# Optimization experiments

Measured on AMD Instinct MI355X. Metric: run time of the kernel, lower is better.

Reference implementation:

```python
import jax, jax.numpy as jnp
import numpy as np
from jax.scipy.special import logsumexp

IN_FEATURES = 1024
N_CLASSES = 50257
CUTOFFS = [4000, 20000, N_CLASSES]  # includes final n_classes, as in the module
SHORTLIST = CUTOFFS[0]
N_CLUSTERS = len(CUTOFFS)
N = 8192


def setup_inputs() -> dict:
    key = jax.random.key(0)
    k1, k2, k3, k4, k5, k6 = jax.random.split(key, 6)
    inp = {
        "input": jax.random.normal(k1, (N, IN_FEATURES), dtype=jnp.float32),
        "target": jax.random.randint(k2, (N,), 0, N_CLASSES, dtype=jnp.int64)
        if jax.config.jax_enable_x64 else jax.random.randint(k2, (N,), 0, N_CLASSES, dtype=jnp.int32),
        # learned parameters
        "weight": jax.random.normal(k3, (N_CLASSES, IN_FEATURES), dtype=jnp.float32) * 0.02,
        "bias": jnp.zeros((N_CLASSES,), dtype=jnp.float32),
        "tail_vectors": jax.random.normal(k4, (N_CLUSTERS - 1, IN_FEATURES), dtype=jnp.float32) * 0.02,
        "tail_bias": jnp.zeros((N_CLUSTERS - 1,), dtype=jnp.float32),
    }
    return inp


def reference(input, target, weight, bias, tail_vectors, tail_bias):
    cutoff_values = [0] + CUTOFFS  # [0, 4000, 20000, 50257]

    # head = shortlist classes + one logit per tail cluster
    head_weight = jnp.concatenate([weight[:SHORTLIST], tail_vectors], axis=0)
    head_bias = jnp.concatenate([bias[:SHORTLIST], tail_bias], axis=0)
    head_logits = input @ head_weight.T + head_bias              # [N, shortlist + n_clusters-1]
    head_logprob = jax.nn.log_softmax(head_logits, axis=1)

    # which cluster each target falls in: 0 = shortlist, 1.. = tails
    boundaries = jnp.asarray(CUTOFFS[:-1])                        # [4000, 20000]
    cluster_id = jnp.searchsorted(boundaries, target, side="right")  # [N]

    # index into head distribution: target itself for shortlist, else cluster logit slot
    gather_inds = jnp.where(cluster_id == 0, target, SHORTLIST + cluster_id - 1)
    head_term = jnp.take_along_axis(head_logprob, gather_inds[:, None], axis=1)[:, 0]

    # per-row target logit against the full table (only used for tail rows)
    target_logit = jnp.sum(input * weight[target], axis=-1) + bias[target]  # [N]

    # tail clusters: within-cluster log-prob of the target = logit - logsumexp(cluster logits)
    tail_term = jnp.zeros_like(head_term)
    for i in range(1, N_CLUSTERS):
        lo, hi = cutoff_values[i], cutoff_values[i + 1]
        cluster_logits = input @ weight[lo:hi].T + bias[lo:hi]    # [N, hi-lo]
        lse = logsumexp(cluster_logits, axis=1)                   # [N]
        tail_term = jnp.where(cluster_id == i, target_logit - lse, tail_term)

    output = head_term + tail_term                                # [N] log-probs of targets
    loss = jnp.mean(-output)
    return output, loss
```

## Files before the change

### kernel.cpp

```cpp
#include <hip/hip_runtime.h>
#include <stddef.h>
#include <stdint.h>

#define IN_F      1024
#define SHORTLIST 4000
#define C1_LO     4000
#define C1_HI     20000
#define C2_HI     50257
#define NROWS     8192

#define WS_CNT1   0
#define WS_CNT2   1
#define WS_LOSS   2
#define WS_RL1    4
#define WS_RL2    (4 + 8192)
#define WS_SEH    (4 + 2*8192)
#define WS_SET    (WS_SEH + 8192)
#define WS_CAP    (WS_SET + 8192)
#define WS_WORDS  (WS_CAP + 8192)

#define WBF_OFF   (262144)
#define XBF_OFF   (WBF_OFF + 103219200)
#define XBF_BYTES ((size_t)NROWS * IN_F * 2)
#define WS_NEEDED (XBF_OFF + XBF_BYTES)

#define GRID_HEAD 512
#define GRID_T1   2048
#define GRID_T2   3840
#define GRID_ALL  (GRID_HEAD + GRID_T1 + GRID_T2)

typedef float          f32x4  __attribute__((ext_vector_type(4)));
typedef __bf16         bf16x8 __attribute__((ext_vector_type(8)));
typedef unsigned short us8    __attribute__((ext_vector_type(8)));
typedef unsigned short ushort_t;

__device__ __forceinline__ unsigned short f2bf(float f) {
    unsigned int u = __float_as_uint(f);
    u += 0x7fffu + ((u >> 16) & 1u);
    return (unsigned short)(u >> 16);
}

__device__ __forceinline__ void gl_lds16(const void* g, void* l) {
    __builtin_amdgcn_global_load_lds(
        (const __attribute__((address_space(1))) void*)g,
        (__attribute__((address_space(3))) void*)l, 16, 0, 0);
}

__global__ void init_ws_k(int* __restrict__ ws) {
    int i = blockIdx.x * 256 + threadIdx.x;
    if (i < WS_WORDS) {
        int v = (i >= WS_RL1 && i < WS_RL1 + 2*8192) ? -1 : 0;
        ws[i] = v;
    }
}

__global__ void compact_rows_k(const int* __restrict__ target, int* __restrict__ ws) {
    int row = blockIdx.x * 256 + threadIdx.x;
    if (row >= NROWS) return;
    int tg = target[row];
    if (tg >= C1_LO) {
        if (tg < C1_HI) {
            int p = atomicAdd(&ws[WS_CNT1], 1);
            ws[WS_RL1 + p] = row;
        } else {
            int p = atomicAdd(&ws[WS_CNT2], 1);
            ws[WS_RL2 + p] = row;
        }
    }
}

#define WCHUNKS ((C2_HI * IN_F) / 8)
#define XCHUNKS ((NROWS * IN_F) / 8)
__global__ void convert_bf16_k(const float* __restrict__ w_src,
                               ushort_t* __restrict__ w_dst,
                               const float* __restrict__ x_src,
                               ushort_t* __restrict__ x_dst) {
    int i = blockIdx.x * 256 + threadIdx.x;
    const float* p;
    ushort_t* d;
    if (i < WCHUNKS) { p = w_src + (size_t)i * 8; d = w_dst + (size_t)i * 8; }
    else {
        int j = i - WCHUNKS;
        if (j >= XCHUNKS) return;
        p = x_src + (size_t)j * 8; d = x_dst + (size_t)j * 8;
    }
    f32x4 x0 = *(const f32x4*)p;
    f32x4 x1 = *(const f32x4*)(p + 4);
    us8 o;
    o[0] = f2bf(x0[0]); o[1] = f2bf(x0[1]); o[2] = f2bf(x0[2]); o[3] = f2bf(x0[3]);
    o[4] = f2bf(x1[0]); o[5] = f2bf(x1[1]); o[6] = f2bf(x1[2]); o[7] = f2bf(x1[3]);
    *(us8*)d = o;
}

__launch_bounds__(256, 3)
__global__ void gemm_lse_fused_k(const ushort_t* __restrict__ Xbf,
                                 const ushort_t* __restrict__ Wbf,
                                 const float* __restrict__ bias,
                                 const int*   __restrict__ target,
                                 int*   __restrict__ wsI,
                                 float* __restrict__ wsF)
{
    const int bid = blockIdx.x;
    int rs, cg, cbase, C, cnt;
    const int* rowlist;
    float* sumexp;
    if (bid < GRID_HEAD) {
        rs = bid & 63; cg = bid >> 6;
        cbase = 0; C = SHORTLIST; rowlist = nullptr; cnt = NROWS;
        sumexp = wsF + WS_SEH;
    } else if (bid < GRID_HEAD + GRID_T1) {
        int b = bid - GRID_HEAD;
        rs = b & 63; cg = b >> 6;
        cbase = C1_LO; C = C1_HI - C1_LO; rowlist = wsI + WS_RL1; cnt = wsI[WS_CNT1];
        sumexp = wsF + WS_SET;
    } else {
        int b = bid - (GRID_HEAD + GRID_T1);
        rs = b & 63; cg = b >> 6;
        cbase = C1_HI; C = C2_HI - C1_HI; rowlist = wsI + WS_RL2; cnt = wsI[WS_CNT2];
        sumexp = wsF + WS_SET;
    }
    const int r0 = rs * 128;
    if (r0 >= cnt) return;
    float* capture = wsF + WS_CAP;

    __shared__ ushort_t As[128 * 64];
    __shared__ ushort_t Bs[128 * 64];
    __shared__ int   orig_s[128];
    __shared__ int   tgt_s[128];
    __shared__ float part[256];

    const int tid = threadIdx.x;
    part[tid] = 0.f;
    if (tid < 128) {
        int idx  = r0 + tid;
        int orig = (idx < cnt) ? (rowlist ? rowlist[idx] : idx) : -1;
        orig_s[tid] = orig;
        tgt_s[tid]  = (orig >= 0) ? target[orig] : -1;
    }
    __syncthreads();

    const int lane = tid & 63;
    const int wave = tid >> 6;
    const int wm = wave >> 1, wn = wave & 1;
    const int q = lane >> 4, s = lane & 15;

    const int lrow  = lane >> 3;
    const int chunk = (lane & 7) ^ lrow;
    const ushort_t* aptr[4];
    ushort_t* alds[4];
    ushort_t* blds[4];
    int brow[4];
#pragma unroll
    for (int i = 0; i < 4; ++i) {
        int t  = wave * 4 + i;
        int rt = t * 8 + lrow;
        int orig = orig_s[rt]; if (orig < 0) orig = 0;
        aptr[i] = Xbf + (size_t)orig * IN_F + chunk * 8;
        alds[i] = &As[t * 512];
        blds[i] = &Bs[t * 512];
        brow[i] = rt;
    }

    int aoff[4], boff[4];
#pragma unroll
    for (int i = 0; i < 4; ++i) {
        aoff[i] = (wm * 64 + i * 16 + s) * 64;
        boff[i] = (wn * 64 + i * 16 + s) * 64;
    }
    const int slot0 = (q ^ (s & 7)) * 8;
    const int slot1 = slot0 ^ (4 * 8);

    for (int ct = 0; ct < 4; ++ct) {
        const int c0 = (cg * 4 + ct) * 128;
        if (c0 >= C) break;

        const ushort_t* bptr[4];
#pragma unroll
        for (int i = 0; i < 4; ++i) {
            int c = c0 + brow[i]; if (c >= C) c = C - 1;
            bptr[i] = Wbf + (size_t)(cbase + c) * IN_F + chunk * 8;
        }

        f32x4 acc[4][4];
#pragma unroll
        for (int mi = 0; mi < 4; ++mi)
#pragma unroll
            for (int ni = 0; ni < 4; ++ni) acc[mi][ni] = (f32x4)0.f;

        for (int k0 = 0; k0 < IN_F; k0 += 64) {
            __syncthreads();
#pragma unroll
            for (int i = 0; i < 4; ++i) {
                gl_lds16(aptr[i] + k0, alds[i]);
                gl_lds16(bptr[i] + k0, blds[i]);
            }
            __syncthreads();

#pragma unroll
            for (int ks = 0; ks < 2; ++ks) {
                const int sl = ks ? slot1 : slot0;
                bf16x8 av[4], bv[4];
#pragma unroll
                for (int i = 0; i < 4; ++i) {
                    av[i] = *(const bf16x8*)&As[aoff[i] + sl];
                    bv[i] = *(const bf16x8*)&Bs[boff[i] + sl];
                }
#pragma unroll
                for (int mi = 0; mi < 4; ++mi)
#pragma unroll
                    for (int ni = 0; ni < 4; ++ni)
                        acc[mi][ni] = __builtin_amdgcn_mfma_f32_16x16x32_bf16(
                            av[mi], bv[ni], acc[mi][ni], 0, 0, 0);
            }
        }

        float bias_v[4];
#pragma unroll
        for (int ni = 0; ni < 4; ++ni) {
            int cgl = c0 + wn * 64 + ni * 16 + s;
            bias_v[ni] = (cgl < C) ? bias[cbase + cgl] : 0.f;
        }
#pragma unroll
        for (int mi = 0; mi < 4; ++mi) {
#pragma unroll
            for (int r = 0; r < 4; ++r) {
                int rl   = wm * 64 + mi * 16 + q * 4 + r;
                int orig = orig_s[rl];
                int tg   = tgt_s[rl];
                float sum = 0.f;
#pragma unroll
                for (int ni = 0; ni < 4; ++ni) {
                    int cgl = c0 + wn * 64 + ni * 16 + s;
                    float logit = acc[mi][ni][r] + bias_v[ni];
                    bool valid = (cgl < C) && (orig >= 0);
                    float e = valid ? __expf(logit) : 0.f;
                    sum += e;
                    if (valid && (cbase + cgl == tg)) capture[orig] = logit;
                }
                sum += __shfl_xor(sum, 1, 64);
                sum += __shfl_xor(sum, 2, 64);
                sum += __shfl_xor(sum, 4, 64);
                sum += __shfl_xor(sum, 8, 64);
                if (s == 0 && orig >= 0) part[wn * 128 + rl] += sum;
            }
        }
    }

    __syncthreads();
    if (tid < 128) {
        int orig = orig_s[tid];
        if (orig >= 0) {
            float tot = part[tid] + part[128 + tid];
            atomicAdd(&sumexp[orig], tot);
        }
    }
}

__launch_bounds__(256)
__global__ void gemm_lse_k(const float* __restrict__ input,
                           const float* __restrict__ weight,
                           const float* __restrict__ bias,
                           const int*   __restrict__ target,
                           const int*   __restrict__ rowlist,
                           const int*   __restrict__ cnt_ptr,
                           int fixed_cnt,
                           int class_base, int C,
                           float* __restrict__ sumexp,
                           float* __restrict__ capture)
{
    const int cnt = cnt_ptr ? *cnt_ptr : fixed_cnt;
    const int r0  = blockIdx.x * 128;
    if (r0 >= cnt) return;
    const int c0  = blockIdx.y * 128;

    __shared__ unsigned short As[128 * 40];
    __shared__ unsigned short Bs[128 * 40];
    __shared__ int   orig_s[128];
    __shared__ int   tgt_s[128];
    __shared__ float bias_s[128];

    const int tid = threadIdx.x;
    if (tid < 128) {
        int idx  = r0 + tid;
        int orig = -1;
        if (idx < cnt) orig = rowlist ? rowlist[idx] : idx;
        orig_s[tid] = orig;
        tgt_s[tid]  = (orig >= 0) ? target[orig] : -1;
        int c = c0 + tid;
        bias_s[tid] = (c < C) ? bias[class_base + c] : 0.f;
    }

    const int lane = tid & 63;
    const int wave = tid >> 6;
    const int wm = wave >> 1, wn = wave & 1;
    const int q = lane >> 4, s = lane & 15;

    int aoff[4], boff[4];
#pragma unroll
    for (int i = 0; i < 4; ++i) {
        aoff[i] = (wm * 64 + i * 16 + s) * 40 + q * 8;
        boff[i] = (wn * 64 + i * 16 + s) * 40 + q * 8;
    }

    f32x4 acc[4][4];
#pragma unroll
    for (int mi = 0; mi < 4; ++mi)
#pragma unroll
        for (int ni = 0; ni < 4; ++ni) acc[mi][ni] = (f32x4)0.f;

    for (int k0 = 0; k0 < IN_F; k0 += 32) {
        __syncthreads();
#pragma unroll
        for (int i = 0; i < 2; ++i) {
            int sg  = tid + i * 256;
            int row = sg >> 2;
            int sk  = (sg & 3) << 3;
            {
                int orig = orig_s[row];
                float v[8];
                if (orig >= 0) {
                    const float* p = input + (size_t)orig * IN_F + k0 + sk;
                    f32x4 x0 = *(const f32x4*)p;
                    f32x4 x1 = *(const f32x4*)(p + 4);
                    v[0]=x0[0]; v[1]=x0[1]; v[2]=x0[2]; v[3]=x0[3];
                    v[4]=x1[0]; v[5]=x1[1]; v[6]=x1[2]; v[7]=x1[3];
                } else {
#pragma unroll
                    for (int j = 0; j < 8; ++j) v[j] = 0.f;
                }
                us8 o;
#pragma unroll
                for (int j = 0; j < 8; ++j) o[j] = f2bf(v[j]);
                *(us8*)&As[row * 40 + sk] = o;
            }
            {
                int c = c0 + row;
                float v[8];
                if (c < C) {
                    const float* p = weight + (size_t)(class_base + c) * IN_F + k0 + sk;
                    f32x4 x0 = *(const f32x4*)p;
                    f32x4 x1 = *(const f32x4*)(p + 4);
                    v[0]=x0[0]; v[1]=x0[1]; v[2]=x0[2]; v[3]=x0[3];
                    v[4]=x1[0]; v[5]=x1[1]; v[6]=x1[2]; v[7]=x1[3];
                } else {
#pragma unroll
                    for (int j = 0; j < 8; ++j) v[j] = 0.f;
                }
                us8 o;
#pragma unroll
                for (int j = 0; j < 8; ++j) o[j] = f2bf(v[j]);
                *(us8*)&Bs[row * 40 + sk] = o;
            }
        }
        __syncthreads();

        bf16x8 av[4], bv[4];
#pragma unroll
        for (int i = 0; i < 4; ++i) {
            av[i] = *(const bf16x8*)&As[aoff[i]];
            bv[i] = *(const bf16x8*)&Bs[boff[i]];
        }
#pragma unroll
        for (int mi = 0; mi < 4; ++mi)
#pragma unroll
            for (int ni = 0; ni < 4; ++ni)
                acc[mi][ni] = __builtin_amdgcn_mfma_f32_16x16x32_bf16(
                    av[mi], bv[ni], acc[mi][ni], 0, 0, 0);
    }

#pragma unroll
    for (int mi = 0; mi < 4; ++mi) {
#pragma unroll
        for (int r = 0; r < 4; ++r) {
            int rl   = wm * 64 + mi * 16 + q * 4 + r;
            int orig = orig_s[rl];
            int tg   = tgt_s[rl];
            float sum = 0.f;
#pragma unroll
            for (int ni = 0; ni < 4; ++ni) {
                int cl = wn * 64 + ni * 16 + s;
                int cg = c0 + cl;
                float logit = acc[mi][ni][r] + bias_s[cl];
                bool valid = (cg < C) && (orig >= 0);
                float e = valid ? __expf(logit) : 0.f;
                sum += e;
                if (valid && (class_base + cg == tg)) capture[orig] = logit;
            }
            sum += __shfl_xor(sum, 1, 64);
            sum += __shfl_xor(sum, 2, 64);
            sum += __shfl_xor(sum, 4, 64);
            sum += __shfl_xor(sum, 8, 64);
            if (s == 0 && orig >= 0) atomicAdd(&sumexp[orig], sum);
        }
    }
}

__global__ void combine_k(const float* __restrict__ input,
                          const int*   __restrict__ target,
                          const float* __restrict__ tv,
                          const float* __restrict__ tb,
                          const float* __restrict__ sumexp_head,
                          const float* __restrict__ sumexp_tail,
                          const float* __restrict__ capture,
                          float* __restrict__ out,
                          float* __restrict__ loss_accum)
{
    const int wave = threadIdx.x >> 6, lane = threadIdx.x & 63;
    const int row = blockIdx.x * 4 + wave;
    if (row >= NROWS) return;

    const float* x  = input + (size_t)row * IN_F + lane * 16;
    const float* p0 = tv + lane * 16;
    const float* p1 = tv + IN_F + lane * 16;
    float d0 = 0.f, d1 = 0.f;
#pragma unroll
    for (int i = 0; i < 16; i += 4) {
        f32x4 xv = *(const f32x4*)(x  + i);
        f32x4 a  = *(const f32x4*)(p0 + i);
        f32x4 b  = *(const f32x4*)(p1 + i);
        d0 += xv[0]*a[0] + xv[1]*a[1] + xv[2]*a[2] + xv[3]*a[3];
        d1 += xv[0]*b[0] + xv[1]*b[1] + xv[2]*b[2] + xv[3]*b[3];
    }
#pragma unroll
    for (int m = 32; m; m >>= 1) {
        d0 += __shfl_xor(d0, m, 64);
        d1 += __shfl_xor(d1, m, 64);
    }
    if (lane == 0) {
        float t0 = d0 + tb[0];
        float t1 = d1 + tb[1];
        int tg  = target[row];
        int cid = (tg < C1_LO) ? 0 : ((tg < C1_HI) ? 1 : 2);
        float se_head  = sumexp_head[row] + __expf(t0) + __expf(t1);
        float lse_head = __logf(se_head);
        float head_num = (cid == 0) ? capture[row] : ((cid == 1) ? t0 : t1);
        float o = head_num - lse_head;
        if (cid != 0) o += capture[row] - __logf(sumexp_tail[row]);
        out[row] = o;
        atomicAdd(loss_accum, o);
    }
}

__global__ void finalize_k(const float* __restrict__ loss_accum, float* __restrict__ out) {
    out[NROWS] = -loss_accum[0] * (1.0f / NROWS);
}

extern "C" void kernel_launch(void* const* d_in, const int* in_sizes, int n_in,
                              void* d_out, int out_size, void* d_ws, size_t ws_size,
                              hipStream_t stream) {
    const float* input  = (const float*)d_in[0];
    const int*   target = (const int*)  d_in[1];
    const float* weight = (const float*)d_in[2];
    const float* bias   = (const float*)d_in[3];
    const float* tv     = (const float*)d_in[4];
    const float* tb     = (const float*)d_in[5];
    float* out = (float*)d_out;
    int*   wsI = (int*)d_ws;
    float* wsF = (float*)d_ws;

    init_ws_k<<<dim3((WS_WORDS + 255) / 256), 256, 0, stream>>>(wsI);
    compact_rows_k<<<dim3(NROWS / 256), 256, 0, stream>>>(target, wsI);

    const bool fast = ws_size >= (size_t)WS_NEEDED;

    if (fast) {
        ushort_t* Wbf = (ushort_t*)((char*)d_ws + WBF_OFF);
        ushort_t* Xbf = (ushort_t*)((char*)d_ws + XBF_OFF);

        convert_bf16_k<<<dim3((WCHUNKS + XCHUNKS + 255) / 256), 256, 0, stream>>>(
            weight, Wbf, input, Xbf);

        gemm_lse_fused_k<<<dim3(GRID_ALL), 256, 0, stream>>>(
            Xbf, Wbf, bias, target, wsI, wsF);
    } else {
        gemm_lse_k<<<dim3(NROWS / 128, (SHORTLIST + 127) / 128), 256, 0, stream>>>(
            input, weight, bias, target,
            nullptr, nullptr, NROWS,
            0, SHORTLIST,
            wsF + WS_SEH, wsF + WS_CAP);
        gemm_lse_k<<<dim3(NROWS / 128, (C1_HI - C1_LO + 127) / 128), 256, 0, stream>>>(
            input, weight, bias, target,
            wsI + WS_RL1, wsI + WS_CNT1, 0,
            C1_LO, C1_HI - C1_LO,
            wsF + WS_SET, wsF + WS_CAP);
        gemm_lse_k<<<dim3(NROWS / 128, (C2_HI - C1_HI + 127) / 128), 256, 0, stream>>>(
            input, weight, bias, target,
            wsI + WS_RL2, wsI + WS_CNT2, 0,
            C1_HI, C2_HI - C1_HI,
            wsF + WS_SET, wsF + WS_CAP);
    }

    combine_k<<<dim3(NROWS / 4), 256, 0, stream>>>(
        input, target, tv, tb,
        wsF + WS_SEH, wsF + WS_SET, wsF + WS_CAP,
        out, wsF + WS_LOSS);

    finalize_k<<<1, 1, 0, stream>>>(wsF + WS_LOSS, out);
}
```

Before: 1.189 ms.

## Double-buffer LDS tiles with vmcnt-gated prefetch in the fused GEMM-LSE kernel

Replaces the single 64-wide K tile, which needed two syncthreads per step, with two 32-wide LDS buffers pairs. The next K slice is loaded asynchronously via global_load_lds while MFMAs consume the current one, using s_waitcnt vmcnt(4) and raw barriers instead of full drains. The LDS swizzle and the thread-to-row mapping are reworked for the 32-element row stride. The aim is to hide global-load latency behind matrix math, at the cost of more barriers per unit of K and a hand-tuned wait count that must match the number of loads issued.

```diff
diff --git a/kernel.cpp b/kernel.cpp
--- a/kernel.cpp
+++ b/kernel.cpp
@@ -45,6 +45,10 @@
         (const __attribute__((address_space(1))) void*)g,
         (__attribute__((address_space(3))) void*)l, 16, 0, 0);
 }
+
+#define VMCNT4() asm volatile("s_waitcnt vmcnt(4)" ::: "memory")
+#define VMCNT0() asm volatile("s_waitcnt vmcnt(0)" ::: "memory")
+#define BAR()    __builtin_amdgcn_s_barrier()
 
 __global__ void init_ws_k(int* __restrict__ ws) {
     int i = blockIdx.x * 256 + threadIdx.x;
@@ -123,8 +127,10 @@
     if (r0 >= cnt) return;
     float* capture = wsF + WS_CAP;
 
-    __shared__ ushort_t As[128 * 64];
-    __shared__ ushort_t Bs[128 * 64];
+    __shared__ ushort_t As0[128 * 32];
+    __shared__ ushort_t Bs0[128 * 32];
+    __shared__ ushort_t As1[128 * 32];
+    __shared__ ushort_t Bs1[128 * 32];
     __shared__ int   orig_s[128];
     __shared__ int   tgt_s[128];
     __shared__ float part[256];
@@ -144,74 +150,60 @@
     const int wm = wave >> 1, wn = wave & 1;
     const int q = lane >> 4, s = lane & 15;
 
-    const int lrow  = lane >> 3;
-    const int chunk = (lane & 7) ^ lrow;
-    const ushort_t* aptr[4];
-    ushort_t* alds[4];
-    ushort_t* blds[4];
-    int brow[4];
+    const int lrow = lane >> 2;
+    const int psw  = (lane & 3) ^ ((lane >> 3) & 3);
+    const ushort_t* aptr[2];
+    int tsl[2];
+    int brow[2];
+#pragma unroll
+    for (int i = 0; i < 2; ++i) {
+        int t  = wave * 2 + i;
+        int rt = t * 16 + lrow;
+        int orig = orig_s[rt]; if (orig < 0) orig = 0;
+        aptr[i] = Xbf + (size_t)orig * IN_F + psw * 8;
+        tsl[i]  = t * 512;
+        brow[i] = rt;
+    }
+
+    int ar_off[4], br_off[4];
 #pragma unroll
     for (int i = 0; i < 4; ++i) {
-        int t  = wave * 4 + i;
-        int rt = t * 8 + lrow;
-        int orig = orig_s[rt]; if (orig < 0) orig = 0;
-        aptr[i] = Xbf + (size_t)orig * IN_F + chunk * 8;
-        alds[i] = &As[t * 512];
-        blds[i] = &Bs[t * 512];
-        brow[i] = rt;
-    }
-
-    int aoff[4], boff[4];
-#pragma unroll
-    for (int i = 0; i < 4; ++i) {
-        aoff[i] = (wm * 64 + i * 16 + s) * 64;
-        boff[i] = (wn * 64 + i * 16 + s) * 64;
-    }
-    const int slot0 = (q ^ (s & 7)) * 8;
-    const int slot1 = slot0 ^ (4 * 8);
+        ar_off[i] = (wm * 64 + i * 16 + s) * 32 + (q ^ ((s >> 1) & 3)) * 8;
+        br_off[i] = (wn * 64 + i * 16 + s) * 32 + (q ^ ((s >> 1) & 3)) * 8;
+    }
+
+#define STAGE(AS, BS, K0) do {                                                 \
+    _Pragma("unroll")                                                          \
+    for (int i_ = 0; i_ < 2; ++i_) {                                           \
+        gl_lds16(aptr[i_] + (K0), &AS[tsl[i_]]);                               \
+        gl_lds16(bptr[i_] + (K0), &BS[tsl[i_]]);                               \
+    }                                                                          \
+} while (0)
+
+#define MFMA_STEP(AS, BS) do {                                                 \
+    bf16x8 av_[4], bv_[4];                                                     \
+    _Pragma("unroll")                                                          \
+    for (int i_ = 0; i_ < 4; ++i_) {                                           \
+        av_[i_] = *(const bf16x8*)&AS[ar_off[i_]];                             \
+        bv_[i_] = *(const bf16x8*)&BS[br_off[i_]];                             \
+    }                                                                          \
+    _Pragma("unroll")                                                          \
+    for (int mi_ = 0; mi_ < 4; ++mi_)                                          \
+        _Pragma("unroll")                                                      \
+        for (int ni_ = 0; ni_ < 4; ++ni_)                                      \
+            acc[mi_][ni_] = __builtin_amdgcn_mfma_f32_16x16x32_bf16(           \
+                av_[mi_], bv_[ni_], acc[mi_][ni_], 0, 0, 0);                   \
+} while (0)
 
     for (int ct = 0; ct < 4; ++ct) {
         const int c0 = (cg * 4 + ct) * 128;
         if (c0 >= C) break;
 
-        const ushort_t* bptr[4];
-#pragma unroll
-        for (int i = 0; i < 4; ++i) {
+        const ushort_t* bptr[2];
+#pragma unroll
+        for (int i = 0; i < 2; ++i) {
             int c = c0 + brow[i]; if (c >= C) c = C - 1;
-            bptr[i] = Wbf + (size_t)(cbase + c) * IN_F + chunk * 8;
-        }
-
-        f32x4 acc[4][4];
-#pragma unroll
-        for (int mi = 0; mi < 4; ++mi)
-#pragma unroll
-            for (int ni = 0; ni < 4; ++ni) acc[mi][ni] = (f32x4)0.f;
-
-        for (int k0 = 0; k0 < IN_F; k0 += 64) {
-            __syncthreads();
-#pragma unroll
-            for (int i = 0; i < 4; ++i) {
-                gl_lds16(aptr[i] + k0, alds[i]);
-                gl_lds16(bptr[i] + k0, blds[i]);
-            }
-            __syncthreads();
-
-#pragma unroll
-            for (int ks = 0; ks < 2; ++ks) {
-                const int sl = ks ? slot1 : slot0;
-                bf16x8 av[4], bv[4];
-#pragma unroll
-                for (int i = 0; i < 4; ++i) {
-                    av[i] = *(const bf16x8*)&As[aoff[i] + sl];
-                    bv[i] = *(const bf16x8*)&Bs[boff[i] + sl];
-                }
-#pragma unroll
-                for (int mi = 0; mi < 4; ++mi)
-#pragma unroll
-                    for (int ni = 0; ni < 4; ++ni)
-                        acc[mi][ni] = __builtin_amdgcn_mfma_f32_16x16x32_bf16(
-                            av[mi], bv[ni], acc[mi][ni], 0, 0, 0);
-            }
+            bptr[i] = Wbf + (size_t)(cbase + c) * IN_F + psw * 8;
         }
 
         float bias_v[4];
@@ -220,6 +212,42 @@
             int cgl = c0 + wn * 64 + ni * 16 + s;
             bias_v[ni] = (cgl < C) ? bias[cbase + cgl] : 0.f;
         }
+
+        f32x4 acc[4][4];
+#pragma unroll
+        for (int mi = 0; mi < 4; ++mi)
+#pragma unroll
+            for (int ni = 0; ni < 4; ++ni) acc[mi][ni] = (f32x4)0.f;
+
+        STAGE(As0, Bs0, 0);
+        VMCNT0();
+        BAR();
+
+        int k = 0;
+        for (int kp = 0; kp < 15; ++kp) {
+            STAGE(As1, Bs1, k + 32);
+            VMCNT4();
+            BAR();
+            MFMA_STEP(As0, Bs0);
+            BAR();
+
+            STAGE(As0, Bs0, k + 64);
+            VMCNT4();
+            BAR();
+            MFMA_STEP(As1, Bs1);
+            BAR();
+            k += 64;
+        }
+
+        STAGE(As1, Bs1, 992);
+        VMCNT4();
+        BAR();
+        MFMA_STEP(As0, Bs0);
+        BAR();
+        VMCNT0();
+        BAR();
+        MFMA_STEP(As1, Bs1);
+
 #pragma unroll
         for (int mi = 0; mi < 4; ++mi) {
 #pragma unroll
@@ -245,6 +273,9 @@
             }
         }
     }
+
+#undef STAGE
+#undef MFMA_STEP
 
     __syncthreads();
     if (tid < 128) {
```

Result: no change. 1.200 ms (+0.9%).
